# Performance work log

Hardware: AMD Instinct MI355X
Metric: run time of the kernel (lower is better)

The kernel has to match this reference:

```python
import jax, jax.numpy as jnp
import numpy as np

D_MODEL = 1024
HEADS = 16
DK = D_MODEL // HEADS
B, S = 2, 2048


def setup_inputs() -> dict:
    key = jax.random.key(0)
    ks = jax.random.split(key, 9)
    s = 0.02
    return {
        "Q": jax.random.normal(ks[0], (B, S, D_MODEL), jnp.float32),
        "K": jax.random.normal(ks[1], (B, S, D_MODEL), jnp.float32),
        "V": jax.random.normal(ks[2], (B, S, D_MODEL), jnp.float32),
        "mask": jnp.ones((B, 1, S), jnp.int32),
        "Wq": jax.random.normal(ks[3], (D_MODEL, D_MODEL), jnp.float32) * s,
        "Wk": jax.random.normal(ks[4], (D_MODEL, D_MODEL), jnp.float32) * s,
        "Wv": jax.random.normal(ks[5], (D_MODEL, D_MODEL), jnp.float32) * s,
        "Wo": jax.random.normal(ks[6], (D_MODEL, D_MODEL), jnp.float32) * s,
        "ln_gamma": jnp.ones((D_MODEL,), jnp.float32),
        "ln_beta": jnp.zeros((D_MODEL,), jnp.float32),
    }


def _layer_norm(x, gamma, beta, eps=1e-5):
    mu = jnp.mean(x, axis=-1, keepdims=True)
    var = jnp.mean(jnp.square(x - mu), axis=-1, keepdims=True)
    return (x - mu) * jax.lax.rsqrt(var + eps) * gamma + beta


def reference(Q, K, V, mask, Wq, Wk, Wv, Wo, ln_gamma, ln_beta):
    # torch Linear(no bias): y = x @ W.T
    def split_heads(x):  # [B,S,D] -> [B,H,S,dk]
        return x.reshape(B, -1, HEADS, DK).transpose(0, 2, 1, 3)

    q = split_heads(Q @ Wq.T)
    k = split_heads(K @ Wk.T)
    v = split_heads(V @ Wv.T)

    # scores: [B,H,Sq,Sk]
    scores = jnp.einsum("bhqd,bhkd->bhqk", q, k) / np.sqrt(DK).astype(np.float32)
    m = mask[:, None, :, :]  # [B,1,1,S] broadcast over heads and queries
    scores = jnp.where(m == 0, -jnp.inf, scores)
    attn = jax.nn.softmax(scores, axis=-1)  # dropout is identity in eval
    out = jnp.einsum("bhqk,bhkd->bhqd", attn, v)
    out = out.transpose(0, 2, 1, 3).reshape(B, -1, D_MODEL)
    out = out @ Wo.T
    return _layer_norm(out + Q, ln_gamma, ln_beta)
```

## Files before the change

### kernel.cpp

```cpp
#include <hip/hip_runtime.h>
#include <hip/hip_bf16.h>
#include <stdint.h>

#define NB 2
#define NS 2048
#define ND 1024
#define NH 16
#define NDK 64
#define NM (NB*NS)

using bf16x8 = __attribute__((ext_vector_type(8))) short;
using f32x4  = __attribute__((ext_vector_type(4))) float;
using f32x16 = __attribute__((ext_vector_type(16))) float;
using u32x4  = __attribute__((ext_vector_type(4))) unsigned;

__device__ __forceinline__ unsigned short f2bf(float f){
  unsigned u = __float_as_uint(f);
  u += 0x7fffu + ((u>>16)&1u);
  return (unsigned short)(u>>16);
}

__device__ __forceinline__ void gload_lds16(const void* g, void* l){
  __builtin_amdgcn_global_load_lds((const __attribute__((address_space(1))) void*)g,
                                   (__attribute__((address_space(3))) void*)l, 16, 0, 0);
}

__device__ __forceinline__ float fexp2(float x){
#if __has_builtin(__builtin_amdgcn_exp2f)
  return __builtin_amdgcn_exp2f(x);
#else
  return __expf(x * 0.69314718056f);
#endif
}

__device__ __forceinline__ unsigned cvtpk_bf16(float lo, float hi){
  unsigned r;
  asm("v_cvt_pk_bf16_f32 %0, %1, %2" : "=v"(r) : "v"(lo), "v"(hi));
  return r;
}

__device__ __forceinline__ void swap32(unsigned &a, unsigned &b){
#if __has_builtin(__builtin_amdgcn_permlane32_swap)
  auto rr = __builtin_amdgcn_permlane32_swap((int)a, (int)b, false, false);
  a = (unsigned)rr[0]; b = (unsigned)rr[1];
#else
  const bool lo = (threadIdx.x & 32) == 0;
  unsigned sa = (unsigned)__shfl_xor((int)a, 32, 64);
  unsigned sb = (unsigned)__shfl_xor((int)b, 32, 64);
  unsigned na = lo ? a : sb;
  unsigned nb = lo ? sa : b;
  a = na; b = nb;
#endif
}

__device__ __forceinline__ f32x16 mfma32(bf16x8 a, bf16x8 b, f32x16 c){
  return __builtin_amdgcn_mfma_f32_32x32x16_bf16(a, b, c, 0, 0, 0);
}

__global__ __launch_bounds__(256) void prep_k(const float* __restrict__ Q, const float* __restrict__ K,
                                              const float* __restrict__ V, const float* __restrict__ Wq,
                                              const float* __restrict__ Wk, const float* __restrict__ Wv,
                                              const float* __restrict__ Wo,
                                              unsigned short* __restrict__ Xbf,
                                              unsigned short* __restrict__ Wbf){
  const int bid = blockIdx.x;
  const float* src; unsigned short* dst; int i;
  if (bid < 12288){
    const int which = bid >> 12;
    src = (which==0) ? Q : (which==1) ? K : V;
    dst = Xbf + ((size_t)which << 22);
    i = (bid & 4095)*256 + threadIdx.x;
  } else {
    const int which = (bid - 12288) >> 10;
    src = (which==0) ? Wq : (which==1) ? Wk : (which==2) ? Wv : Wo;
    dst = Wbf + ((size_t)which << 20);
    i = ((bid - 12288) & 1023)*256 + threadIdx.x;
  }
  float4 v = ((const float4*)src)[i];
  ushort4 o;
  o.x = f2bf(v.x); o.y = f2bf(v.y); o.z = f2bf(v.z); o.w = f2bf(v.w);
  ((ushort4*)dst)[i] = o;
}

__global__ __launch_bounds__(256) void gemm_qkv(const short* __restrict__ Xbf, const short* __restrict__ Wbf,
                                                unsigned short* __restrict__ qh, unsigned short* __restrict__ kh,
                                                unsigned short* __restrict__ vT){
  __shared__ short lsA[2][4096];
  __shared__ short lsB[2][4096];
  const int tid = threadIdx.x;
  const int hw = blockIdx.x;
  const int logical = (hw & 7)*96 + (hw >> 3);
  const int z = logical >> 8, rem = logical & 255;
  const int my = rem >> 3, nx = rem & 7;
  const short* A = Xbf + (size_t)z*NM*ND;
  const short* W = Wbf + (size_t)z*ND*ND;
  unsigned short* out = (z==0) ? qh : (z==1) ? kh : vT;
  const int mode = (z==2) ? 1 : 0;
  const int m0 = my*128, n0 = nx*128;

  const short* gA = A + (size_t)m0*1024;
  const short* gB = W + (size_t)n0*1024;
  const int srow = tid>>2, scol = (tid&3)*8;
  const int w = tid>>6, lane = tid&63, lr = lane&15, lk = lane>>4;
  const int wm = w>>1, wn = w&1;

  f32x4 acc[4][4];
  #pragma unroll
  for (int i=0;i<4;++i)
    #pragma unroll
    for (int j=0;j<4;++j) acc[i][j] = (f32x4){0.f,0.f,0.f,0.f};

  #pragma unroll
  for (int r=0;r<2;++r){
    gload_lds16(gA + (size_t)(r*64+srow)*1024 + scol, &lsA[0][(r*256+tid)*8]);
    gload_lds16(gB + (size_t)(r*64+srow)*1024 + scol, &lsB[0][(r*256+tid)*8]);
  }
  int cur = 0;
  for (int ks=0; ks<32; ++ks){
    __syncthreads();
    if (ks+1 < 32){
      const int k0 = (ks+1)*32;
      #pragma unroll
      for (int r=0;r<2;++r){
        gload_lds16(gA + (size_t)(r*64+srow)*1024 + k0 + scol, &lsA[cur^1][(r*256+tid)*8]);
        gload_lds16(gB + (size_t)(r*64+srow)*1024 + k0 + scol, &lsB[cur^1][(r*256+tid)*8]);
      }
    }
    bf16x8 af[4], bfr[4];
    #pragma unroll
    for (int i=0;i<4;++i){
      af[i]  = *(const bf16x8*)&lsA[cur][(wm*64+i*16+lr)*32 + lk*8];
      bfr[i] = *(const bf16x8*)&lsB[cur][(wn*64+i*16+lr)*32 + lk*8];
    }
    #pragma unroll
    for (int i=0;i<4;++i)
      #pragma unroll
      for (int j=0;j<4;++j)
        acc[i][j] = __builtin_amdgcn_mfma_f32_16x16x32_bf16(af[i], bfr[j], acc[i][j], 0,0,0);
    cur ^= 1;
  }
  #pragma unroll
  for (int i=0;i<4;++i)
    #pragma unroll
    for (int j=0;j<4;++j)
      #pragma unroll
      for (int r=0;r<4;++r){
        const int m = m0 + wm*64 + i*16 + lk*4 + r;
        const int n = n0 + wn*64 + j*16 + lr;
        const float v = acc[i][j][r];
        const int b = m>>11, s = m&2047, h = n>>6, dk = n&63;
        size_t addr;
        if (mode == 0) addr = (((size_t)(b*NH+h))*NS + s)*NDK + dk;
        else           addr = (((size_t)(b*NH+h))*NDK + dk)*NS + s;
        out[addr] = f2bf(v);
      }
}

__global__ __launch_bounds__(256) void gemm_out(const short* __restrict__ Attn, const short* __restrict__ Wo,
                                                const float* __restrict__ Qin, float* __restrict__ proj){
  __shared__ short lsA[2][4096];
  __shared__ short lsB[2][4096];
  const int tid = threadIdx.x;
  const int hw = blockIdx.x;
  const int logical = (hw & 7)*32 + (hw >> 3);
  const int my = logical >> 3, nx = logical & 7;
  const int m0 = my*128, n0 = nx*128;
  const short* gA = Attn + (size_t)m0*1024;
  const short* gB = Wo + (size_t)n0*1024;
  const int srow = tid>>2, scol = (tid&3)*8;
  const int w = tid>>6, lane = tid&63, lr = lane&15, lk = lane>>4;
  const int wm = w>>1, wn = w&1;

  f32x4 acc[4][4];
  #pragma unroll
  for (int i=0;i<4;++i)
    #pragma unroll
    for (int j=0;j<4;++j) acc[i][j] = (f32x4){0.f,0.f,0.f,0.f};

  #pragma unroll
  for (int r=0;r<2;++r){
    gload_lds16(gA + (size_t)(r*64+srow)*1024 + scol, &lsA[0][(r*256+tid)*8]);
    gload_lds16(gB + (size_t)(r*64+srow)*1024 + scol, &lsB[0][(r*256+tid)*8]);
  }
  int cur = 0;
  for (int ks=0; ks<32; ++ks){
    __syncthreads();
    if (ks+1 < 32){
      const int k0 = (ks+1)*32;
      #pragma unroll
      for (int r=0;r<2;++r){
        gload_lds16(gA + (size_t)(r*64+srow)*1024 + k0 + scol, &lsA[cur^1][(r*256+tid)*8]);
        gload_lds16(gB + (size_t)(r*64+srow)*1024 + k0 + scol, &lsB[cur^1][(r*256+tid)*8]);
      }
    }
    bf16x8 af[4], bfr[4];
    #pragma unroll
    for (int i=0;i<4;++i){
      af[i]  = *(const bf16x8*)&lsA[cur][(wm*64+i*16+lr)*32 + lk*8];
      bfr[i] = *(const bf16x8*)&lsB[cur][(wn*64+i*16+lr)*32 + lk*8];
    }
    #pragma unroll
    for (int i=0;i<4;++i)
      #pragma unroll
      for (int j=0;j<4;++j)
        acc[i][j] = __builtin_amdgcn_mfma_f32_16x16x32_bf16(af[i], bfr[j], acc[i][j], 0,0,0);
    cur ^= 1;
  }
  #pragma unroll
  for (int i=0;i<4;++i)
    #pragma unroll
    for (int j=0;j<4;++j)
      #pragma unroll
      for (int r=0;r<4;++r){
        const int m = m0 + wm*64 + i*16 + lk*4 + r;
        const int n = n0 + wn*64 + j*16 + lr;
        proj[(size_t)m*1024 + n] = acc[i][j][r] + Qin[(size_t)m*1024 + n];
      }
}

__global__ __launch_bounds__(512) void attn_k(const short* __restrict__ qh, const short* __restrict__ kh,
                                              const short* __restrict__ vT, const int* __restrict__ mask,
                                              unsigned short* __restrict__ attn){
  __shared__ char sb[66048];
  const int bid = blockIdx.x;
  const int qb = bid & 15, h = (bid>>4)&15, b = bid>>8;
  const int tid = threadIdx.x, w = tid>>6, lane = tid&63;
  const int ql = lane & 31, hi = lane>>5;
  const int qw = w & 3, half = w>>2;
  const int bh = b*NH + h;
  const int q0 = qb*128 + qw*32;
  const float C2 = 0.18033688f;

  const int D = tid*16;
  const int strow = D>>7;
  const int S = D ^ ((strow&7)<<4);
  const char* ksrc = (const char*)(kh + (size_t)bh*NS*NDK) + S;
  const char* vsrc = (const char*)(vT + ((size_t)bh*NDK + strow)*NS) + (S & 127);

  const short* qrow = qh + ((size_t)bh*NS + q0 + ql)*NDK + hi*8;
  bf16x8 qf[4];
  #pragma unroll
  for (int kp=0;kp<4;++kp) qf[kp] = *(const bf16x8*)(qrow + kp*16);

  const int* mrow = mask + b*NS;
  unsigned long long* smask = (unsigned long long*)(sb + 65536);

  gload_lds16(ksrc,                      sb + D);
  gload_lds16(ksrc + (size_t)1024*128,   sb + 8192 + D);
  gload_lds16(vsrc,                      sb + 32768 + D);
  gload_lds16(vsrc + (size_t)1024*2,     sb + 32768 + 8192 + D);

  #pragma unroll
  for (int j=0;j<4;++j){
    const int gt = w*4 + j;
    const unsigned long long bal = __ballot(mrow[gt*64 + lane] != 0);
    if (lane == 0) smask[gt] = bal;
  }

  f32x16 o0, o1;
  #pragma unroll
  for (int r=0;r<16;++r){ o0[r]=0.f; o1[r]=0.f; }
  float mrun = -1e30f, lrun = 0.f;

  const int swz = (ql&7)<<4;

  for (int t=0; t<16; ++t){
    const int buf = (t&1)*16384;
    __syncthreads();
    if (t+1 < 16){
      const int nbuf = ((t+1)&1)*16384;
      const size_t kvn0 = (size_t)(t+1)*64, kvn1 = 1024 + kvn0;
      gload_lds16(ksrc + kvn0*128, sb + nbuf + D);
      gload_lds16(ksrc + kvn1*128, sb + nbuf + 8192 + D);
      gload_lds16(vsrc + kvn0*2,   sb + 32768 + nbuf + D);
      gload_lds16(vsrc + kvn1*2,   sb + 32768 + nbuf + 8192 + D);
    }
    const unsigned long long m64 = smask[half*16 + t];
    const unsigned mw0 = (unsigned)m64, mw1 = (unsigned)(m64>>32);
    const bool allm = (~m64) == 0ull;

    const char* kb = sb + buf + half*8192;
    const char* vb = sb + 32768 + buf + half*8192;

    bf16x8 kf[8];
    #pragma unroll
    for (int kvh=0;kvh<2;++kvh)
      #pragma unroll
      for (int kp=0;kp<4;++kp)
        kf[kvh*4+kp] = *(const bf16x8*)(kb + (((kvh*32+ql)*128 + kp*32 + hi*16) ^ swz));

    f32x16 s0, s1;
    #pragma unroll
    for (int r=0;r<16;++r){ s0[r]=0.f; s1[r]=0.f; }
    #pragma unroll
    for (int kp=0;kp<4;++kp){
      s0 = mfma32(kf[kp],   qf[kp], s0);
      s1 = mfma32(kf[4+kp], qf[kp], s1);
    }

    float t16[16];
    #pragma unroll
    for (int r=0;r<16;++r) t16[r] = fmaxf(s0[r], s1[r]);
    #pragma unroll
    for (int st=8; st>=1; st>>=1)
      #pragma unroll
      for (int r=0;r<st;++r) t16[r] = fmaxf(t16[r], t16[r+st]);
    const float tm = fmaxf(t16[0], __shfl_xor(t16[0], 32, 64));

    if (!__all(tm - mrun <= 32.f)){
      const float mnew = fmaxf(mrun, tm);
      const float fac  = fexp2((mrun - mnew)*C2);
      mrun = mnew;
      #pragma unroll
      for (int r=0;r<16;++r){ o0[r]*=fac; o1[r]*=fac; }
      lrun *= fac;
    }
    const float nb = mrun*C2;

    bf16x8 vf[8];
    #pragma unroll
    for (int dh=0;dh<2;++dh)
      #pragma unroll
      for (int c=0;c<4;++c)
        vf[dh*4+c] = *(const bf16x8*)(vb + (((dh*32+ql)*128 + c*32 + hi*16) ^ swz));

    float psum = 0.f;
    #pragma unroll
    for (int kvh=0; kvh<2; ++kvh){
      const f32x16& ss = kvh ? s1 : s0;
      const unsigned mw = kvh ? mw1 : mw0;
      unsigned pwd[8];
      float ps0 = 0.f, ps1 = 0.f;
      #pragma unroll
      for (int i=0;i<8;++i){
        const int bp0 = ((2*i)&3) + 8*((2*i)>>2);
        float p0 = fexp2(ss[2*i]*C2   - nb);
        float p1 = fexp2(ss[2*i+1]*C2 - nb);
        if (!allm){
          p0 = ((mw >> (bp0     + 4*hi)) & 1u) ? p0 : 0.f;
          p1 = ((mw >> (bp0 + 1 + 4*hi)) & 1u) ? p1 : 0.f;
        }
        ps0 += p0; ps1 += p1;
        pwd[i] = cvtpk_bf16(p0, p1);
      }
      psum += ps0 + ps1;
      swap32(pwd[0], pwd[2]);
      swap32(pwd[1], pwd[3]);
      swap32(pwd[4], pwd[6]);
      swap32(pwd[5], pwd[7]);
      u32x4 c0w = {pwd[0], pwd[1], pwd[2], pwd[3]};
      u32x4 c1w = {pwd[4], pwd[5], pwd[6], pwd[7]};
      bf16x8 pf0 = __builtin_bit_cast(bf16x8, c0w);
      bf16x8 pf1 = __builtin_bit_cast(bf16x8, c1w);
      o0 = mfma32(vf[2*kvh],       pf0, o0);
      o1 = mfma32(vf[4 + 2*kvh],   pf0, o1);
      o0 = mfma32(vf[2*kvh + 1],   pf1, o0);
      o1 = mfma32(vf[4 + 2*kvh+1], pf1, o1);
    }
    psum += __shfl_xor(psum, 32, 64);
    lrun += psum;
  }

  __syncthreads();
  float* smm = (float*)(sb + 32768);
  float* sml = (float*)(sb + 32768 + 1024);
  if (hi == 0){ smm[w*32 + ql] = mrun; sml[w*32 + ql] = lrun; }
  __syncthreads();
  const float pmv = smm[(w^4)*32 + ql], plv = sml[(w^4)*32 + ql];
  const float mfin = fmaxf(mrun, pmv);
  const float facS = fexp2((mrun - mfin)*C2);
  if (w >= 4){
    float* eg = (float*)(sb + (size_t)(w-4)*8192);
    #pragma unroll
    for (int r=0;r<16;++r){
      eg[ql + 32*(hi*16 + r)]        = o0[r]*facS;
      eg[ql + 32*(hi*16 + r) + 1024] = o1[r]*facS;
    }
  }
  __syncthreads();
  if (w < 4){
    float* eg = (float*)(sb + (size_t)w*8192);
    #pragma unroll
    for (int r=0;r<16;++r){
      o0[r] = o0[r]*facS + eg[ql + 32*(hi*16 + r)];
      o1[r] = o1[r]*facS + eg[ql + 32*(hi*16 + r) + 1024];
    }
    const float facP = fexp2((pmv - mfin)*C2);
    const float lfin = lrun*facS + plv*facP;
    const float inv = 1.f / lfin;
    asm volatile("s_waitcnt lgkmcnt(0)" ::: "memory");
    char* ep = sb + (size_t)w*8192;
    #pragma unroll
    for (int dh=0; dh<2; ++dh){
      const f32x16& oo = dh ? o1 : o0;
      #pragma unroll
      for (int i=0;i<8;++i){
        const int d0 = ((2*i)&3) + 8*((2*i)>>2) + 4*hi + dh*32;
        const unsigned pk = cvtpk_bf16(oo[2*i]*inv, oo[2*i+1]*inv);
        *(unsigned*)(ep + (((ql*128) + d0*2) ^ ((ql&7)<<4))) = pk;
      }
    }
    asm volatile("s_waitcnt lgkmcnt(0)" ::: "memory");
    #pragma unroll
    for (int seg=0; seg<4; ++seg){
      const int qq = seg*8 + (lane>>3), dc = (lane&7)*8;
      bf16x8 vv = *(const bf16x8*)(ep + (((qq*128) + dc*2) ^ ((qq&7)<<4)));
      *(bf16x8*)(attn + ((size_t)b*NS + q0 + qq)*ND + h*NDK + dc) = vv;
    }
  }
}

__global__ __launch_bounds__(256) void ln_k(const float* __restrict__ proj,
                                            const float* __restrict__ gamma, const float* __restrict__ beta,
                                            float* __restrict__ out){
  const int row = blockIdx.x*4 + (threadIdx.x>>6);
  const int lane = threadIdx.x & 63;
  const float4* pp = (const float4*)(proj + (size_t)row*ND);
  float4 x[4];
  float sum = 0.f;
  #pragma unroll
  for (int i=0;i<4;++i){
    x[i] = pp[lane + i*64];
    sum += x[i].x + x[i].y + x[i].z + x[i].w;
  }
  #pragma unroll
  for (int off=32; off>=1; off>>=1) sum += __shfl_xor(sum, off, 64);
  const float mu = sum * (1.f/1024.f);
  float vs = 0.f;
  #pragma unroll
  for (int i=0;i<4;++i){
    float d0=x[i].x-mu, d1=x[i].y-mu, d2=x[i].z-mu, d3=x[i].w-mu;
    vs += d0*d0 + d1*d1 + d2*d2 + d3*d3;
  }
  #pragma unroll
  for (int off=32; off>=1; off>>=1) vs += __shfl_xor(vs, off, 64);
  const float rstd = rsqrtf(vs*(1.f/1024.f) + 1e-5f);
  #pragma unroll
  for (int i=0;i<4;++i){
    const float4 g  = ((const float4*)gamma)[lane + i*64];
    const float4 be = ((const float4*)beta)[lane + i*64];
    float4 y;
    y.x = (x[i].x-mu)*rstd*g.x + be.x;
    y.y = (x[i].y-mu)*rstd*g.y + be.y;
    y.z = (x[i].z-mu)*rstd*g.z + be.z;
    y.w = (x[i].w-mu)*rstd*g.w + be.w;
    ((float4*)(out + (size_t)row*ND))[lane + i*64] = y;
  }
}

extern "C" void kernel_launch(void* const* d_in, const int* in_sizes, int n_in,
                              void* d_out, int out_size, void* d_ws, size_t ws_size,
                              hipStream_t stream){
  const float* Q    = (const float*)d_in[0];
  const float* K    = (const float*)d_in[1];
  const float* V    = (const float*)d_in[2];
  const int*   mask = (const int*)  d_in[3];
  const float* Wq   = (const float*)d_in[4];
  const float* Wk   = (const float*)d_in[5];
  const float* Wv   = (const float*)d_in[6];
  const float* Wo   = (const float*)d_in[7];
  const float* gam  = (const float*)d_in[8];
  const float* bet  = (const float*)d_in[9];
  float* out = (float*)d_out;
  char* ws = (char*)d_ws;

  unsigned short* Wbf  = (unsigned short*)(ws);
  unsigned short* Xbf  = (unsigned short*)(ws + (size_t)(8u<<20));
  unsigned short* qhp  = (unsigned short*)(ws + (size_t)(32u<<20));
  unsigned short* khp  = (unsigned short*)(ws + (size_t)(40u<<20));
  unsigned short* vTp  = (unsigned short*)(ws + (size_t)(48u<<20));
  unsigned short* attb = (unsigned short*)(ws + (size_t)(56u<<20));
  float* proj  = (float*)(ws + (size_t)(8u<<20));

  prep_k<<<16384,256,0,stream>>>(Q, K, V, Wq, Wk, Wv, Wo, Xbf, Wbf);

  gemm_qkv<<<768,256,0,stream>>>((const short*)Xbf, (const short*)Wbf, qhp, khp, vTp);

  attn_k<<<512,512,0,stream>>>((const short*)qhp, (const short*)khp, (const short*)vTp, mask, attb);

  gemm_out<<<256,256,0,stream>>>((const short*)attb, (const short*)(Wbf + (3u<<20)), Q, proj);

  ln_k<<<1024,256,0,stream>>>(proj, gam, bet, out);
}
```

Baseline: 173.2 us.

## Swizzle GEMM LDS tiles, remap attention blocks, inline mask ballot, add MFMA priority

The two GEMM kernels now XOR-swizzle the 16-byte column chunk by row in both the global-to-LDS stores and the fragment reads, to reduce LDS bank conflicts. The attention kernel remaps block IDs so that consecutive hardware blocks in groups of eight cover different query blocks and heads, likely to spread work across XCDs and share K/V in cache. It also drops the precomputed shared-memory mask bitmap and computes the ballot per tile from global memory. The MFMA sections are wrapped in s_setprio raises so matrix issue wins arbitration over other waves. The extra global mask loads inside the loop could add latency.

```diff
diff --git a/kernel.cpp b/kernel.cpp
--- a/kernel.cpp
+++ b/kernel.cpp
@@ -100,7 +100,8 @@
 
   const short* gA = A + (size_t)m0*1024;
   const short* gB = W + (size_t)n0*1024;
-  const int srow = tid>>2, scol = (tid&3)*8;
+  const int srow = tid>>2;
+  const int scol = ((tid&3)*8) ^ (((srow>>1)&3)<<3);
   const int w = tid>>6, lane = tid&63, lr = lane&15, lk = lane>>4;
   const int wm = w>>1, wn = w&1;
 
@@ -127,10 +128,14 @@
       }
     }
     bf16x8 af[4], bfr[4];
+    const char* Ab = (const char*)&lsA[cur][0];
+    const char* Bb = (const char*)&lsB[cur][0];
     #pragma unroll
     for (int i=0;i<4;++i){
-      af[i]  = *(const bf16x8*)&lsA[cur][(wm*64+i*16+lr)*32 + lk*8];
-      bfr[i] = *(const bf16x8*)&lsB[cur][(wn*64+i*16+lr)*32 + lk*8];
+      const int ra = wm*64 + i*16 + lr;
+      const int rb = wn*64 + i*16 + lr;
+      af[i]  = *(const bf16x8*)(Ab + ra*64 + ((lk*16) ^ (((ra>>1)&3)<<4)));
+      bfr[i] = *(const bf16x8*)(Bb + rb*64 + ((lk*16) ^ (((rb>>1)&3)<<4)));
     }
     #pragma unroll
     for (int i=0;i<4;++i)
@@ -167,7 +172,8 @@
   const int m0 = my*128, n0 = nx*128;
   const short* gA = Attn + (size_t)m0*1024;
   const short* gB = Wo + (size_t)n0*1024;
-  const int srow = tid>>2, scol = (tid&3)*8;
+  const int srow = tid>>2;
+  const int scol = ((tid&3)*8) ^ (((srow>>1)&3)<<3);
   const int w = tid>>6, lane = tid&63, lr = lane&15, lk = lane>>4;
   const int wm = w>>1, wn = w&1;
 
@@ -194,10 +200,14 @@
       }
     }
     bf16x8 af[4], bfr[4];
+    const char* Ab = (const char*)&lsA[cur][0];
+    const char* Bb = (const char*)&lsB[cur][0];
     #pragma unroll
     for (int i=0;i<4;++i){
-      af[i]  = *(const bf16x8*)&lsA[cur][(wm*64+i*16+lr)*32 + lk*8];
-      bfr[i] = *(const bf16x8*)&lsB[cur][(wn*64+i*16+lr)*32 + lk*8];
+      const int ra = wm*64 + i*16 + lr;
+      const int rb = wn*64 + i*16 + lr;
+      af[i]  = *(const bf16x8*)(Ab + ra*64 + ((lk*16) ^ (((ra>>1)&3)<<4)));
+      bfr[i] = *(const bf16x8*)(Bb + rb*64 + ((lk*16) ^ (((rb>>1)&3)<<4)));
     }
     #pragma unroll
     for (int i=0;i<4;++i)
@@ -221,9 +231,10 @@
 __global__ __launch_bounds__(512) void attn_k(const short* __restrict__ qh, const short* __restrict__ kh,
                                               const short* __restrict__ vT, const int* __restrict__ mask,
                                               unsigned short* __restrict__ attn){
-  __shared__ char sb[66048];
-  const int bid = blockIdx.x;
-  const int qb = bid & 15, h = (bid>>4)&15, b = bid>>8;
+  __shared__ char sb[65536];
+  const int hw = blockIdx.x;
+  const int logical = (hw & 7)*64 + (hw >> 3);
+  const int qb = logical & 15, h = (logical>>4)&15, b = logical>>8;
   const int tid = threadIdx.x, w = tid>>6, lane = tid&63;
   const int ql = lane & 31, hi = lane>>5;
   const int qw = w & 3, half = w>>2;
@@ -242,20 +253,12 @@
   #pragma unroll
   for (int kp=0;kp<4;++kp) qf[kp] = *(const bf16x8*)(qrow + kp*16);
 
-  const int* mrow = mask + b*NS;
-  unsigned long long* smask = (unsigned long long*)(sb + 65536);
+  const int* mrow = mask + b*NS + half*1024;
 
   gload_lds16(ksrc,                      sb + D);
   gload_lds16(ksrc + (size_t)1024*128,   sb + 8192 + D);
   gload_lds16(vsrc,                      sb + 32768 + D);
   gload_lds16(vsrc + (size_t)1024*2,     sb + 32768 + 8192 + D);
-
-  #pragma unroll
-  for (int j=0;j<4;++j){
-    const int gt = w*4 + j;
-    const unsigned long long bal = __ballot(mrow[gt*64 + lane] != 0);
-    if (lane == 0) smask[gt] = bal;
-  }
 
   f32x16 o0, o1;
   #pragma unroll
@@ -275,9 +278,9 @@
       gload_lds16(vsrc + kvn0*2,   sb + 32768 + nbuf + D);
       gload_lds16(vsrc + kvn1*2,   sb + 32768 + nbuf + 8192 + D);
     }
-    const unsigned long long m64 = smask[half*16 + t];
-    const unsigned mw0 = (unsigned)m64, mw1 = (unsigned)(m64>>32);
-    const bool allm = (~m64) == 0ull;
+    const unsigned long long bal = __ballot(mrow[t*64 + lane] != 0);
+    const unsigned mw0 = (unsigned)bal, mw1 = (unsigned)(bal>>32);
+    const bool allm = (~bal) == 0ull;
 
     const char* kb = sb + buf + half*8192;
     const char* vb = sb + 32768 + buf + half*8192;
@@ -292,11 +295,13 @@
     f32x16 s0, s1;
     #pragma unroll
     for (int r=0;r<16;++r){ s0[r]=0.f; s1[r]=0.f; }
+    __builtin_amdgcn_s_setprio(1);
     #pragma unroll
     for (int kp=0;kp<4;++kp){
       s0 = mfma32(kf[kp],   qf[kp], s0);
       s1 = mfma32(kf[4+kp], qf[kp], s1);
     }
+    __builtin_amdgcn_s_setprio(0);
 
     float t16[16];
     #pragma unroll
@@ -352,10 +357,12 @@
       u32x4 c1w = {pwd[4], pwd[5], pwd[6], pwd[7]};
       bf16x8 pf0 = __builtin_bit_cast(bf16x8, c0w);
       bf16x8 pf1 = __builtin_bit_cast(bf16x8, c1w);
+      __builtin_amdgcn_s_setprio(1);
       o0 = mfma32(vf[2*kvh],       pf0, o0);
       o1 = mfma32(vf[4 + 2*kvh],   pf0, o1);
       o0 = mfma32(vf[2*kvh + 1],   pf1, o0);
       o1 = mfma32(vf[4 + 2*kvh+1], pf1, o1);
+      __builtin_amdgcn_s_setprio(0);
     }
     psum += __shfl_xor(psum, 32, 64);
     lrun += psum;
```

Result: faster. 168.9 us (-2.5%).
